# Performance work log

Measured on AMD Instinct MI355X. Metric: run time of the kernel, lower is better.

## Reference

```python
import jax, jax.numpy as jnp
import numpy as np

B, H, W, C = 16, 48, 48, 256
D_INNER = 2 * C          # ssm_ratio = 2.0
D_STATE = 1
DT_RANK = C // 16        # mamba convention: dt_rank = d_model // 16
HID = 4 * C              # mlp_ratio = 4.0
N = H * W


def _grid_neighbors(h, w):
    idx = np.arange(h * w).reshape(h, w)
    pad_r = -np.ones((1, w), np.int64)
    pad_c = -np.ones((h, 1), np.int64)
    up = np.concatenate([pad_r, idx[:-1]], 0)
    down = np.concatenate([idx[1:], pad_r], 0)
    left = np.concatenate([pad_c, idx[:, :-1]], 1)
    right = np.concatenate([idx[:, 1:], pad_c], 1)
    nb = np.stack([up, down, left, right], -1).reshape(h * w, 4)
    valid = nb >= 0
    return jnp.asarray(np.where(valid, nb, 0), np.int32), jnp.asarray(valid)

_NBR, _VALID = _grid_neighbors(H, W)


def _mst(x):
    """Input-adaptive MST (Prim) on the 4-connected pixel grid.
    Edge weight = exp(1 - cosine_similarity) between adjacent pixel features.
    Returns (order, par): Prim insertion order (a valid BFS-like topological order:
    every node's parent appears earlier) and parent node id per node."""
    b = x.shape[0]
    f = x.reshape(b, N, C)
    f = f / (jnp.linalg.norm(f, axis=-1, keepdims=True) + 1e-8)
    cos = jnp.einsum('bnc,bnkc->bnk', f, f[:, _NBR])          # (B,N,4)
    wgt = jnp.where(_VALID, jnp.exp(1.0 - cos), jnp.inf)

    def prim(wb):
        key = jnp.full((N,), jnp.inf, wb.dtype).at[0].set(0.0)
        par = jnp.zeros((N,), jnp.int32)
        intree = jnp.zeros((N,), bool)

        def step(carry, _):
            key, par, intree = carry
            u = jnp.argmin(jnp.where(intree, jnp.inf, key)).astype(jnp.int32)
            intree = intree.at[u].set(True)
            nb, wv = _NBR[u], wb[u]
            better = (~intree[nb]) & (wv < key[nb])
            key = key.at[nb].set(jnp.where(better, wv, key[nb]))
            par = par.at[nb].set(jnp.where(better, u, par[nb]))
            return (key, par, intree), u

        (_, par, _), order = jax.lax.scan(step, (key, par, intree), None, length=N)
        return order, par

    return jax.vmap(prim)(wgt)


def _ln(x, g, b):
    m = jnp.mean(x, -1, keepdims=True)
    v = jnp.var(x, -1, keepdims=True)
    return (x - m) * jax.lax.rsqrt(v + 1e-5) * g + b


def _tree_ssm(xn, order, par, W_in, b_in, W_xp, W_dt, b_dt, A_log, Dp, W_out, b_out):
    """Mamba-style selective scan generalized to a tree: the hidden state of node v
    recurses from its MST parent instead of the previous sequence position."""
    b = xn.shape[0]
    xf = xn.reshape(b, N, C)
    xz = xf @ W_in + b_in                               # (B,N,2*D_INNER)
    xi, z = xz[..., :D_INNER], xz[..., D_INNER:]
    xi = jax.nn.silu(xi)
    dbc = xi @ W_xp                                     # (B,N,DT_RANK+2)
    dtr = dbc[..., :DT_RANK]
    Bv = dbc[..., DT_RANK:DT_RANK + 1]                  # d_state = 1
    Cv = dbc[..., DT_RANK + 1:DT_RANK + 2]
    dt = jax.nn.softplus(dtr @ W_dt + b_dt)             # (B,N,D_INNER)
    A = -jnp.exp(A_log)                                 # (D_INNER,)
    decay = jnp.exp(dt * A)
    Bx = dt * Bv * xi

    def tree_scan(ob, pb, db, xb):
        def step(hbuf, v):
            hv = db[v] * hbuf[pb[v]] + xb[v]            # h[v] = decay*h[parent] + B*x
            return hbuf.at[v].set(hv), None
        hbuf, _ = jax.lax.scan(step, jnp.zeros((N, D_INNER), db.dtype), ob)
        return hbuf

    h = jax.vmap(tree_scan)(order, par, decay, Bx)      # (B,N,D_INNER)
    y = Cv * h + Dp * xi
    return ((y * jax.nn.silu(z)) @ W_out + b_out).reshape(xn.shape)


def setup_inputs():
    key = jax.random.key(0)
    ks = jax.random.split(key, 8)
    g = lambda k, shp, s=0.02: jax.random.normal(k, shp, jnp.float32) * s
    return {
        "x": jax.random.normal(ks[0], (B, H, W, C), jnp.float32),
        "norm1_w": jnp.ones((C,), jnp.float32), "norm1_b": jnp.zeros((C,), jnp.float32),
        "norm2_w": jnp.ones((C,), jnp.float32), "norm2_b": jnp.zeros((C,), jnp.float32),
        "W_in": g(ks[1], (C, 2 * D_INNER)), "b_in": jnp.zeros((2 * D_INNER,), jnp.float32),
        "W_xp": g(ks[2], (D_INNER, DT_RANK + 2 * D_STATE)),
        "W_dt": g(ks[3], (DT_RANK, D_INNER), 0.1), "b_dt": jnp.full((D_INNER,), -2.0, jnp.float32),
        "A_log": jnp.zeros((D_INNER,), jnp.float32), "Dp": jnp.ones((D_INNER,), jnp.float32),
        "W_out": g(ks[4], (D_INNER, C)), "b_out": jnp.zeros((C,), jnp.float32),
        "fc1_w": g(ks[5], (C, HID)), "fc1_b": jnp.zeros((HID,), jnp.float32),
        "fc2_w": g(ks[6], (HID, C)), "fc2_b": jnp.zeros((C,), jnp.float32),
    }


def reference(x, norm1_w, norm1_b, norm2_w, norm2_b, W_in, b_in, W_xp, W_dt, b_dt,
              A_log, Dp, W_out, b_out, fc1_w, fc1_b, fc2_w, fc2_b):
    order, par = _mst(jax.lax.stop_gradient(x))         # torch.no_grad() MST
    x = x + _tree_ssm(_ln(x, norm1_w, norm1_b), order, par,
                      W_in, b_in, W_xp, W_dt, b_dt, A_log, Dp, W_out, b_out)
    h = jax.nn.gelu(_ln(x, norm2_w, norm2_b) @ fc1_w + fc1_b, approximate=False)
    return x + h @ fc2_w + fc2_b
```

## Files before the change

### kernel.cpp

```cpp
#include <hip/hip_runtime.h>
#include <math.h>

#define NN 2304
#define BB 16
#define CC 256
#define DI 512
#define MM (BB*NN)

typedef __attribute__((ext_vector_type(8))) short bf16x8;
typedef __attribute__((ext_vector_type(4))) float f32x4;

__device__ inline unsigned short f2b(float f){
  unsigned u = __float_as_uint(f);
  u = u + 0x7FFFu + ((u>>16)&1u);
  return (unsigned short)(u>>16);
}
__device__ inline float b2f(unsigned short s){ return __uint_as_float(((unsigned)s)<<16); }
__device__ __forceinline__ int dstep(int d){ return (d==0)?-48:(d==1)?48:(d==2)?-1:1; }

__global__ __launch_bounds__(256) void k_prep(const float* __restrict__ W_in, const float* __restrict__ W_out,
    const float* __restrict__ fc1_w, const float* __restrict__ fc2_w, const float* __restrict__ W_xp,
    unsigned short* __restrict__ WinT, unsigned short* __restrict__ WoutT,
    unsigned short* __restrict__ fc1T, unsigned short* __restrict__ fc2T, float* __restrict__ WxpT)
{
  int idx = blockIdx.x*256 + threadIdx.x;
  if (idx < 262144){ int r=idx>>10, c=idx&1023; WinT[(size_t)c*256 + r] = f2b(W_in[idx]); return; }
  idx -= 262144;
  if (idx < 131072){ int r=idx>>8, c=idx&255; WoutT[(size_t)c*512 + r] = f2b(W_out[idx]); return; }
  idx -= 131072;
  if (idx < 262144){ int r=idx>>10, c=idx&1023; fc1T[(size_t)c*256 + r] = f2b(fc1_w[idx]); return; }
  idx -= 262144;
  if (idx < 262144){ int r=idx>>8, c=idx&255; fc2T[(size_t)c*1024 + r] = f2b(fc2_w[idx]); return; }
  idx -= 262144;
  if (idx < 9216){ int r=idx/18, c=idx-r*18; WxpT[(size_t)c*512 + r] = W_xp[idx]; }
}

__global__ __launch_bounds__(256) void k_normln(const float* __restrict__ xin, const float* __restrict__ g,
    const float* __restrict__ bta, float* __restrict__ innorm, unsigned short* __restrict__ outb)
{
  int row = blockIdx.x*4 + (threadIdx.x>>6); int lane=threadIdx.x&63;
  float4 v = *(const float4*)(xin + (size_t)row*CC + lane*4);
  float sq = v.x*v.x + v.y*v.y + v.z*v.z + v.w*v.w;
  float s  = v.x+v.y+v.z+v.w;
  #pragma unroll
  for (int o=32;o;o>>=1){ sq += __shfl_xor(sq,o); s += __shfl_xor(s,o); }
  if (lane==0) innorm[row] = 1.0f/(sqrtf(sq)+1e-8f);
  float m = s*(1.0f/256.0f);
  float dx=v.x-m, dy=v.y-m, dz=v.z-m, dw=v.w-m;
  float ss=dx*dx+dy*dy+dz*dz+dw*dw;
  #pragma unroll
  for (int o=32;o;o>>=1) ss += __shfl_xor(ss,o);
  float rs = rsqrtf(ss*(1.0f/256.0f)+1e-5f);
  int cb=lane*4;
  unsigned o0 = (unsigned)f2b(dx*rs*g[cb+0]+bta[cb+0]) | ((unsigned)f2b(dy*rs*g[cb+1]+bta[cb+1])<<16);
  unsigned o1 = (unsigned)f2b(dz*rs*g[cb+2]+bta[cb+2]) | ((unsigned)f2b(dw*rs*g[cb+3]+bta[cb+3])<<16);
  *(uint2*)(outb + (size_t)row*CC + cb) = make_uint2(o0,o1);
}

__global__ __launch_bounds__(256) void k_edge(const float* __restrict__ x, const float* __restrict__ innorm, float* __restrict__ wgt){
  int g = blockIdx.x*4 + (threadIdx.x>>6); int lane = threadIdx.x&63;
  int b = g/NN, n = g - b*NN;
  int r = n/48, c = n - (n/48)*48;
  const float* xb = x + ((size_t)b*NN)*CC;
  float4 vu = *(const float4*)(xb + (size_t)n*CC + lane*4);
  int nb0=(r>0)?n-48:-1, nb1=(r<47)?n+48:-1, nb2=(c>0)?n-1:-1, nb3=(c<47)?n+1:-1;
  float d0=0,d1=0,d2=0,d3=0;
  if (nb0>=0){ float4 t=*(const float4*)(xb+(size_t)nb0*CC+lane*4); d0=vu.x*t.x+vu.y*t.y+vu.z*t.z+vu.w*t.w; }
  if (nb1>=0){ float4 t=*(const float4*)(xb+(size_t)nb1*CC+lane*4); d1=vu.x*t.x+vu.y*t.y+vu.z*t.z+vu.w*t.w; }
  if (nb2>=0){ float4 t=*(const float4*)(xb+(size_t)nb2*CC+lane*4); d2=vu.x*t.x+vu.y*t.y+vu.z*t.z+vu.w*t.w; }
  if (nb3>=0){ float4 t=*(const float4*)(xb+(size_t)nb3*CC+lane*4); d3=vu.x*t.x+vu.y*t.y+vu.z*t.z+vu.w*t.w; }
  #pragma unroll
  for (int o=32;o;o>>=1){ d0+=__shfl_xor(d0,o); d1+=__shfl_xor(d1,o); d2+=__shfl_xor(d2,o); d3+=__shfl_xor(d3,o); }
  if (lane==0){
    float inu = innorm[g];
    float inf_ = __uint_as_float(0x7F800000u);
    float4 w;
    w.x = (nb0>=0)? expf(1.0f - d0*(inu*innorm[g-n+nb0])) : inf_;
    w.y = (nb1>=0)? expf(1.0f - d1*(inu*innorm[g-n+nb1])) : inf_;
    w.z = (nb2>=0)? expf(1.0f - d2*(inu*innorm[g-n+nb2])) : inf_;
    w.w = (nb3>=0)? expf(1.0f - d3*(inu*innorm[g-n+nb3])) : inf_;
    *(float4*)(wgt + (size_t)g*4) = w;
  }
}

#define INFB 0x7F800000u
#define NILA 0x3FFFu
__device__ void mst_body(unsigned char* smem, const float* __restrict__ wgt, int b,
    unsigned short* __restrict__ parpos_g, int* __restrict__ lvlorder,
    int* __restrict__ lvlstart, int* __restrict__ nlvl)
{
  unsigned* tmask = (unsigned*)smem;
  unsigned* pk    = (unsigned*)(smem + 9216);
  unsigned* comp   = pk;
  unsigned* bestw  = pk + 2304;
  unsigned* bestid = pk + 4608;
  unsigned short* par   = (unsigned short*)(smem + 46080);
  unsigned short* dpos  = (unsigned short*)(smem + 50688);
  int* hist = (int*)(smem + 55296);
  int* ctr  = (int*)(smem + 64512);
  const int tid = threadIdx.x;
  const float* wb = wgt + (size_t)b*NN*4;

  #pragma unroll
  for (int k=0;k<9;k++){ int v=tid+k*256; comp[v]=v; tmask[v]=0u; }
  __syncthreads();

  for (int round=0; round<14; round++){
    #pragma unroll
    for (int k=0;k<9;k++){ int v=tid+k*256; bestw[v]=INFB; bestid[v]=0xFFFFFFFFu; }
    __syncthreads();
    unsigned candw[9], candi[9];
    #pragma unroll
    for (int k=0;k<9;k++){
      int v=tid+k*256;
      unsigned cv=comp[v];
      int r=v/48, c=v-(v/48)*48;
      float4 w4 = *(const float4*)(wb + (size_t)v*4);
      unsigned cw=INFB, ci=0xFFFFFFFFu;
      if (r>0  && comp[v-48]!=cv){ unsigned wv=__float_as_uint(w4.x); if (wv<cw){cw=wv;ci=(unsigned)(v*4+0);} }
      if (r<47 && comp[v+48]!=cv){ unsigned wv=__float_as_uint(w4.y); if (wv<cw){cw=wv;ci=(unsigned)(v*4+1);} }
      if (c>0  && comp[v-1] !=cv){ unsigned wv=__float_as_uint(w4.z); if (wv<cw){cw=wv;ci=(unsigned)(v*4+2);} }
      if (c<47 && comp[v+1] !=cv){ unsigned wv=__float_as_uint(w4.w); if (wv<cw){cw=wv;ci=(unsigned)(v*4+3);} }
      candw[k]=cw; candi[k]=ci;
      if (cw!=INFB) atomicMin(&bestw[cv], cw);
    }
    __syncthreads();
    #pragma unroll
    for (int k=0;k<9;k++){
      if (candw[k]!=INFB){
        int v=tid+k*256; unsigned cv=comp[v];
        if (bestw[cv]==candw[k]) atomicMin(&bestid[cv], candi[k]);
      }
    }
    __syncthreads();
    unsigned hookS[9];
    #pragma unroll
    for (int k=0;k<9;k++){
      int v=tid+k*256; hookS[k]=0xFFFFFFFFu;
      if (comp[v]!=(unsigned)v) continue;
      unsigned id=bestid[v];
      if (id==0xFFFFFFFFu) continue;
      int u=(int)(id>>2), d=(int)(id&3);
      int o = u + dstep(d);
      unsigned s = comp[o];
      unsigned sid = bestid[s];
      bool mutual=false;
      if (sid!=0xFFFFFFFFu){
        int su=(int)(sid>>2), sd=(int)(sid&3);
        int so = su + dstep(sd);
        mutual = (comp[so]==(unsigned)v);
      }
      if (!mutual || (unsigned)v>s) hookS[k]=s;
    }
    __syncthreads();
    #pragma unroll
    for (int k=0;k<9;k++){
      if (hookS[k]==0xFFFFFFFFu) continue;
      int v=tid+k*256;
      unsigned id=bestid[v];
      int u=(int)(id>>2), d=(int)(id&3);
      int o = u + dstep(d);
      comp[v]=hookS[k];
      atomicOr(&tmask[u], 1u<<d);
      atomicOr(&tmask[o], 1u<<(d^1));
    }
    __syncthreads();
    for (int it=0; it<16; it++){
      if (tid==0) ctr[1]=0;
      __syncthreads();
      int ch=0;
      #pragma unroll
      for (int k=0;k<9;k++){
        int v=tid+k*256;
        unsigned c1=comp[v], c2=comp[c1];
        if (c1!=c2){ comp[v]=c2; ch=1; }
      }
      if (ch) atomicAdd(&ctr[1],1);
      __syncthreads();
      if (ctr[1]==0) break;
    }
    if (tid==0) ctr[2]=0;
    __syncthreads();
    int rc=0;
    #pragma unroll
    for (int k=0;k<9;k++){ int v=tid+k*256; if (comp[v]==(unsigned)v) rc++; }
    if (rc) atomicAdd(&ctr[2], rc);
    __syncthreads();
    if (ctr[2]<=1) break;
  }
  __syncthreads();

  int a0;
  { unsigned m0 = tmask[0]; a0 = __ffs((int)(m0&0xFu))-1; }

  for (int pass=0; pass<2; pass++){
    for (int k=0;k<36;k++){
      int a = k*256+tid;
      int v = a>>2, d = a&3;
      unsigned mv = tmask[v];
      unsigned sc = NILA;
      unsigned vl = pass ? 8192u : 0u;
      if ((mv>>d)&1u){
        int w = v + dstep(d);
        unsigned mw = tmask[w];
        int rd = d^1;
        int nd = -1;
        #pragma unroll
        for (int kk=1;kk<=4;kk++){ int c2=(rd+kk)&3; if (nd<0 && ((mw>>c2)&1u)) nd=c2; }
        sc = (unsigned)(w*4+nd);
        if (sc==(unsigned)a0) sc=NILA;
        vl = pass ? (8192u + (((mv>>(4+d))&1u)? 1u : (unsigned)-1)) : 1u;
      }
      pk[a] = (sc<<14) | (vl & 0x3FFFu);
    }
    __syncthreads();
    for (int it=0; it<13; it++){
      unsigned stg[36];
      #pragma unroll
      for (int k=0;k<36;k++){
        int a=k*256+tid;
        unsigned mine=pk[a];
        unsigned s=mine>>14;
        if (s==NILA) stg[k]=mine;
        else {
          unsigned oth=pk[s];
          unsigned nv=(mine&0x3FFFu)+(oth&0x3FFFu);
          if (pass) nv -= 8192u;
          stg[k]=((oth>>14)<<14)|(nv&0x3FFFu);
        }
      }
      __syncthreads();
      #pragma unroll
      for (int k=0;k<36;k++) pk[k*256+tid]=stg[k];
      __syncthreads();
    }
    if (pass==0){
      for (int k=0;k<36;k++){
        int a=k*256+tid;
        int v=a>>2, d=a&3;
        if ((tmask[v]>>d)&1u){
          int w=v+dstep(d);
          int ra=w*4+(d^1);
          if ((pk[a]&0x3FFFu) > (pk[ra]&0x3FFFu)){
            atomicOr(&tmask[v], 16u<<d);
            par[w]=(unsigned short)v;
          }
        }
      }
      __syncthreads();
    }
  }
  if (tid==0){ par[0]=0; dpos[0]=0; ctr[3]=0; }
  __syncthreads();
  for (int k=0;k<36;k++){
    int a=k*256+tid;
    int v=a>>2, d=a&3;
    unsigned mv=tmask[v];
    if (((mv>>d)&1u) && ((mv>>(4+d))&1u)){
      int w=v+dstep(d);
      int S=(int)(pk[a]&0x3FFFu)-8192;
      int dep=1-S;
      dpos[w]=(unsigned short)dep;
      atomicMax(&ctr[3],dep);
    }
  }
  __syncthreads();
  int nlv_=ctr[3]+1;
  for (int i=tid;i<nlv_;i+=256) hist[i]=0;
  __syncthreads();
  for (int i=tid;i<NN;i+=256) atomicAdd(&hist[dpos[i]],1);
  __syncthreads();
  if (tid==0){
    int run=0;
    for (int l=0;l<nlv_;l++){ int c2=hist[l]; hist[l]=run; lvlstart[b*(NN+2)+l]=run; run+=c2; }
    lvlstart[b*(NN+2)+nlv_]=run;
    nlvl[b]=nlv_;
  }
  __syncthreads();
  for (int i=tid;i<NN;i+=256){
    int pos=atomicAdd(&hist[dpos[i]],1);
    lvlorder[b*NN+pos]=i;
    dpos[i]=(unsigned short)pos;
  }
  __syncthreads();
  for (int i=tid;i<NN;i+=256)
    parpos_g[b*NN + dpos[i]] = dpos[par[i]];
}

template<int EPI>
__device__ void gemm_body(unsigned short* lA, unsigned short* lB, int bm, int bn,
    const unsigned short* __restrict__ A, const unsigned short* __restrict__ BT,
    const float* __restrict__ bias, int Ndim, int K,
    const float* __restrict__ addin, float* __restrict__ fout,
    unsigned short* __restrict__ bout0, unsigned short* __restrict__ bout1,
    const int* __restrict__ lvl)
{
  int tid=threadIdx.x, wid=tid>>6, lane=tid&63;
  const unsigned short* Ab = A + (size_t)bm*128*K;
  const unsigned short* Bb = BT + (size_t)bn*128*K;
  int wr=wid>>1, wc=wid&1;
  f32x4 acc[4][4];
  #pragma unroll
  for (int m2=0;m2<4;m2++)
    #pragma unroll
    for (int n2=0;n2<4;n2++)
      #pragma unroll
      for (int j=0;j<4;j++) acc[m2][n2][j]=0.f;
  int r0 = tid>>2, c0 = (tid&3)*8;
  for (int k0=0;k0<K;k0+=32){
    int4 va0 = *(const int4*)(Ab + (size_t)r0*K + k0 + c0);
    int4 va1 = *(const int4*)(Ab + (size_t)(r0+64)*K + k0 + c0);
    int4 vb0 = *(const int4*)(Bb + (size_t)r0*K + k0 + c0);
    int4 vb1 = *(const int4*)(Bb + (size_t)(r0+64)*K + k0 + c0);
    __syncthreads();
    *(int4*)(lA + r0*32 + c0) = va0;
    *(int4*)(lA + (r0+64)*32 + c0) = va1;
    *(int4*)(lB + r0*32 + c0) = vb0;
    *(int4*)(lB + (r0+64)*32 + c0) = vb1;
    __syncthreads();
    int ra = (wr<<6) + (lane&15);
    int rb = (wc<<6) + (lane&15);
    int cb = (lane>>4)<<3;
    bf16x8 af[4], bfr[4];
    #pragma unroll
    for (int m2=0;m2<4;m2++) af[m2] = *(const bf16x8*)(lA + (ra+m2*16)*32 + cb);
    #pragma unroll
    for (int n2=0;n2<4;n2++) bfr[n2] = *(const bf16x8*)(lB + (rb+n2*16)*32 + cb);
    #pragma unroll
    for (int m2=0;m2<4;m2++)
      #pragma unroll
      for (int n2=0;n2<4;n2++)
        acc[m2][n2] = __builtin_amdgcn_mfma_f32_16x16x32_bf16(af[m2], bfr[n2], acc[m2][n2], 0,0,0);
  }
  int rr = (lane>>4)<<2, cc = lane&15;
  #pragma unroll
  for (int m2=0;m2<4;m2++){
    #pragma unroll
    for (int n2=0;n2<4;n2++){
      int col = (bn<<7) + (wc<<6) + (n2<<4) + cc;
      float bs = bias[col];
      #pragma unroll
      for (int j=0;j<4;j++){
        int row = (bm<<7) + (wr<<6) + (m2<<4) + rr + j;
        float v = acc[m2][n2][j] + bs;
        if (EPI==0){
          float sv = v * (1.0f/(1.0f+expf(-v)));
          if (col < DI) bout0[(size_t)row*DI + col] = f2b(sv);
          else          bout1[(size_t)row*DI + col - DI] = f2b(sv);
        } else if (EPI==1){
          size_t oi=(size_t)row*Ndim+col;
          fout[oi] = addin[oi] + v;
        } else if (EPI==2){
          size_t oi=(size_t)row*Ndim+col;
          bout0[oi] = f2b(0.5f*v*(1.0f+erff(v*0.70710678118f)));
        } else if (EPI==3){
          int grow = (row/NN)*NN + lvl[row];
          fout[(size_t)row*Ndim+col] = addin[(size_t)grow*Ndim+col] + v;
        } else {
          int grow = (row/NN)*NN + lvl[row];
          fout[(size_t)grow*Ndim+col] = addin[(size_t)row*Ndim+col] + v;
        }
      }
    }
  }
}

template<int EPI>
__global__ __launch_bounds__(256) void k_gemm(
    const unsigned short* __restrict__ A, const unsigned short* __restrict__ BT,
    const float* __restrict__ bias, int Ndim, int K,
    const float* __restrict__ addin, float* __restrict__ fout,
    unsigned short* __restrict__ bout0, unsigned short* __restrict__ bout1,
    const int* __restrict__ lvl)
{
  __shared__ __align__(16) unsigned short lAB[128*32*2];
  int ntn = Ndim>>7;
  int bm = blockIdx.x/ntn, bn = blockIdx.x - bm*ntn;
  gemm_body<EPI>(lAB, lAB+128*32, bm, bn, A, BT, bias, Ndim, K, addin, fout, bout0, bout1, lvl);
}

__global__ __launch_bounds__(256) void k_fused(
    const unsigned short* __restrict__ xn, const unsigned short* __restrict__ WinT,
    const float* __restrict__ b_in,
    unsigned short* __restrict__ xi_b, unsigned short* __restrict__ sz_b,
    const float* __restrict__ wgt, unsigned short* __restrict__ parpos_g,
    int* __restrict__ lvlorder, int* __restrict__ lvlstart, int* __restrict__ nlvl)
{
  __shared__ __align__(16) unsigned char smem[64528];
  if (blockIdx.x < BB){
    mst_body(smem, wgt, blockIdx.x, parpos_g, lvlorder, lvlstart, nlvl);
  } else {
    int bid = blockIdx.x - BB;
    int bm = bid>>3, bn = bid&7;
    gemm_body<0>((unsigned short*)smem, (unsigned short*)smem + 128*32, bm, bn,
                 xn, WinT, b_in, 1024, 256, nullptr, nullptr, xi_b, sz_b, nullptr);
  }
}

__global__ __launch_bounds__(256) void k_ln(const float* __restrict__ xin, const float* __restrict__ g,
    const float* __restrict__ bta, unsigned short* __restrict__ outb)
{
  int row = blockIdx.x*4 + (threadIdx.x>>6); int lane=threadIdx.x&63;
  float4 v = *(const float4*)(xin + (size_t)row*CC + lane*4);
  float s = v.x+v.y+v.z+v.w;
  #pragma unroll
  for (int o=32;o;o>>=1) s += __shfl_xor(s,o);
  float m = s*(1.0f/256.0f);
  float dx=v.x-m, dy=v.y-m, dz=v.z-m, dw=v.w-m;
  float ss=dx*dx+dy*dy+dz*dz+dw*dw;
  #pragma unroll
  for (int o=32;o;o>>=1) ss += __shfl_xor(ss,o);
  float rs = rsqrtf(ss*(1.0f/256.0f)+1e-5f);
  int cb=lane*4;
  unsigned o0 = (unsigned)f2b(dx*rs*g[cb+0]+bta[cb+0]) | ((unsigned)f2b(dy*rs*g[cb+1]+bta[cb+1])<<16);
  unsigned o1 = (unsigned)f2b(dz*rs*g[cb+2]+bta[cb+2]) | ((unsigned)f2b(dw*rs*g[cb+3]+bta[cb+3])<<16);
  *(uint2*)(outb + (size_t)row*CC + cb) = make_uint2(o0,o1);
}

__global__ __launch_bounds__(256) void k_dbc(const unsigned short* __restrict__ xi_b,
    const float* __restrict__ WxpT, float* __restrict__ dbc)
{
  int row = blockIdx.x*4 + (threadIdx.x>>6); int lane=threadIdx.x&63;
  int4 raw = *(const int4*)(xi_b + (size_t)row*DI + lane*8);
  float xf[8];
  xf[0]=b2f((unsigned short)((unsigned)raw.x&0xFFFFu)); xf[1]=b2f((unsigned short)((unsigned)raw.x>>16));
  xf[2]=b2f((unsigned short)((unsigned)raw.y&0xFFFFu)); xf[3]=b2f((unsigned short)((unsigned)raw.y>>16));
  xf[4]=b2f((unsigned short)((unsigned)raw.z&0xFFFFu)); xf[5]=b2f((unsigned short)((unsigned)raw.z>>16));
  xf[6]=b2f((unsigned short)((unsigned)raw.w&0xFFFFu)); xf[7]=b2f((unsigned short)((unsigned)raw.w>>16));
  for (int jc=0;jc<18;jc++){
    const float* wr_ = WxpT + (size_t)jc*DI + lane*8;
    float s=0.f;
    #pragma unroll
    for (int t=0;t<8;t++) s += xf[t]*wr_[t];
    #pragma unroll
    for (int o=32;o;o>>=1) s += __shfl_xor(s,o);
    if (lane==0) dbc[(size_t)row*18+jc]=s;
  }
}

__global__ __launch_bounds__(512) void k_dbx(const float* __restrict__ dbc, const unsigned short* __restrict__ xi_b,
  const float* __restrict__ W_dt, const float* __restrict__ b_dt, const float* __restrict__ A_log,
  const int* __restrict__ lvlorder,
  unsigned short* __restrict__ dec_cm, unsigned short* __restrict__ bx_cm)
{
  __shared__ int smap[32];
  __shared__ float sd[32][18];
  int c = threadIdx.x;
  int b = blockIdx.x/72, pg = blockIdx.x - b*72;
  int p0 = pg*32;
  if (c<32) smap[c] = b*NN + lvlorder[b*NN + p0 + c];
  __syncthreads();
  for (int i=c;i<32*18;i+=512){ int rr=i/18, q=i-rr*18; sd[rr][q]=dbc[(size_t)smap[rr]*18+q]; }
  __syncthreads();
  float wdt[16];
  #pragma unroll
  for (int r2=0;r2<16;r2++) wdt[r2]=W_dt[r2*DI+c];
  float bd=b_dt[c];
  float nA=-expf(A_log[c]);
  unsigned decp[16], bxp[16];
  #pragma unroll
  for (int rr=0;rr<32;rr++){
    float a=bd;
    #pragma unroll
    for (int r2=0;r2<16;r2++) a += sd[rr][r2]*wdt[r2];
    float dt = (a>20.f)? a : log1pf(expf(a));
    float dec = expf(dt*nA);
    float bx = dt*sd[rr][16]*b2f(xi_b[(size_t)smap[rr]*DI + c]);
    if (rr&1){ decp[rr>>1] |= ((unsigned)f2b(dec))<<16; bxp[rr>>1] |= ((unsigned)f2b(bx))<<16; }
    else     { decp[rr>>1]  =  (unsigned)f2b(dec);      bxp[rr>>1]  =  (unsigned)f2b(bx); }
  }
  size_t chb = ((size_t)b*DI + c)*NN + p0;
  uint4* dp = (uint4*)(dec_cm + chb);
  uint4* bp = (uint4*)(bx_cm + chb);
  #pragma unroll
  for (int q=0;q<4;q++){
    uint4 dv, bv;
    dv.x=decp[q*4+0]; dv.y=decp[q*4+1]; dv.z=decp[q*4+2]; dv.w=decp[q*4+3];
    bv.x=bxp[q*4+0];  bv.y=bxp[q*4+1];  bv.z=bxp[q*4+2];  bv.w=bxp[q*4+3];
    dp[q]=dv; bp[q]=bv;
  }
}

#define SCH 4
__global__ __launch_bounds__(256) void k_scan(const unsigned short* __restrict__ dec_cm,
    unsigned short* __restrict__ bx_cm,
    const unsigned short* __restrict__ parpos_g,
    const int* __restrict__ lvlstart, const int* __restrict__ nlvl)
{
  __shared__ unsigned short sdec[SCH*NN];
  __shared__ unsigned short sbx[SCH*NN];
  __shared__ unsigned short spp[NN];
  int b = blockIdx.x>>7, t = blockIdx.x&127;
  int c0 = t*SCH;
  int tid = threadIdx.x;
  const size_t gch = ((size_t)b*DI + c0)*NN;
  #pragma unroll
  for (int cc=0;cc<SCH;cc++){
    const uint2* gd = (const uint2*)(dec_cm + gch + (size_t)cc*NN);
    const uint2* gb = (const uint2*)(bx_cm + gch + (size_t)cc*NN);
    uint2* ld = (uint2*)(sdec + cc*NN);
    uint2* lb = (uint2*)(sbx + cc*NN);
    for (int i=tid;i<NN/4;i+=256){ ld[i]=gd[i]; lb[i]=gb[i]; }
  }
  for (int i=tid;i<NN;i+=256) spp[i]=parpos_g[b*NN+i];
  int nlv = nlvl[b];
  __syncthreads();
  for (int lvl=1; lvl<nlv; lvl++){
    int s=lvlstart[b*(NN+2)+lvl], e=lvlstart[b*(NN+2)+lvl+1];
    int tot=(e-s)*SCH;
    for (int idx=tid; idx<tot; idx+=256){
      int p = s + (idx>>2);
      int cc = idx&3;
      int pp = spp[p];
      float hv = b2f(sdec[cc*NN+p])*b2f(sbx[cc*NN+pp]) + b2f(sbx[cc*NN+p]);
      sbx[cc*NN+p] = f2b(hv);
    }
    __syncthreads();
  }
  #pragma unroll
  for (int cc=0;cc<SCH;cc++){
    uint2* gb = (uint2*)(bx_cm + gch + (size_t)cc*NN);
    const uint2* lb = (const uint2*)(sbx + cc*NN);
    for (int i=tid;i<NN/4;i+=256) gb[i]=lb[i];
  }
}

__global__ __launch_bounds__(512) void k_u(const unsigned short* __restrict__ h_cm,
    const unsigned short* __restrict__ xi_b, const unsigned short* __restrict__ sz_b,
    const float* __restrict__ dbc, const float* __restrict__ Dp,
    const int* __restrict__ lvlorder, unsigned short* __restrict__ u_perm)
{
  __shared__ int smap[32];
  __shared__ unsigned short hT[32*512];
  int c = threadIdx.x;
  int b = blockIdx.x/72, pg = blockIdx.x - b*72;
  int p0 = pg*32;
  if (c<32) smap[c] = b*NN + lvlorder[b*NN + p0 + c];
  {
    const uint4* gh = (const uint4*)(h_cm + ((size_t)b*DI + c)*NN + p0);
    #pragma unroll
    for (int q=0;q<4;q++){
      uint4 w = gh[q];
      unsigned ws[4] = {w.x,w.y,w.z,w.w};
      #pragma unroll
      for (int e=0;e<4;e++){
        hT[(q*8+e*2+0)*512 + c] = (unsigned short)(ws[e]&0xFFFFu);
        hT[(q*8+e*2+1)*512 + c] = (unsigned short)(ws[e]>>16);
      }
    }
  }
  float dpc = Dp[c];
  __syncthreads();
  #pragma unroll 4
  for (int rr=0;rr<32;rr++){
    int grow = smap[rr];
    float Cv = dbc[(size_t)grow*18+17];
    float xiv = b2f(xi_b[(size_t)grow*DI + c]);
    float szv = b2f(sz_b[(size_t)grow*DI + c]);
    float hv = b2f(hT[rr*512 + c]);
    float u = (Cv*hv + dpc*xiv)*szv;
    u_perm[((size_t)(b*NN + p0 + rr))*DI + c] = f2b(u);
  }
}

extern "C" void kernel_launch(void* const* d_in, const int* in_sizes, int n_in,
                              void* d_out, int out_size, void* d_ws, size_t ws_size,
                              hipStream_t stream) {
  (void)in_sizes; (void)n_in; (void)out_size; (void)ws_size;
  const float* x      = (const float*)d_in[0];
  const float* n1w    = (const float*)d_in[1];
  const float* n1b    = (const float*)d_in[2];
  const float* n2w    = (const float*)d_in[3];
  const float* n2b    = (const float*)d_in[4];
  const float* W_in   = (const float*)d_in[5];
  const float* b_in   = (const float*)d_in[6];
  const float* W_xp   = (const float*)d_in[7];
  const float* W_dt   = (const float*)d_in[8];
  const float* b_dt   = (const float*)d_in[9];
  const float* A_log  = (const float*)d_in[10];
  const float* Dp     = (const float*)d_in[11];
  const float* W_out  = (const float*)d_in[12];
  const float* b_out  = (const float*)d_in[13];
  const float* fc1_w  = (const float*)d_in[14];
  const float* fc1_b  = (const float*)d_in[15];
  const float* fc2_w  = (const float*)d_in[16];
  const float* fc2_b  = (const float*)d_in[17];

  char* base=(char*)d_ws; size_t off=0;
  auto alc=[&](size_t nb)->char*{ char* p=base+off; off=(off+nb+255)&~(size_t)255; return p; };
  float* wgt            = (float*)alc((size_t)MM*4*4);
  float* innorm         = (float*)alc((size_t)MM*4);
  unsigned short* parpos= (unsigned short*)alc((size_t)MM*2);
  int* lvlorder         = (int*)alc((size_t)MM*4);
  int* lvlstart         = (int*)alc((size_t)BB*(NN+2)*4);
  int* nlvl             = (int*)alc((size_t)BB*4);
  unsigned short* xi_b  = (unsigned short*)alc((size_t)MM*DI*2);
  unsigned short* sz_b  = (unsigned short*)alc((size_t)MM*DI*2);
  float* dbc            = (float*)alc((size_t)MM*18*4);
  unsigned short* dec_cm= (unsigned short*)alc((size_t)MM*DI*2);
  unsigned short* bx_cm = (unsigned short*)alc((size_t)MM*DI*2);
  unsigned short* WinT  = (unsigned short*)alc((size_t)CC*1024*2);
  unsigned short* WoutT = (unsigned short*)alc((size_t)DI*CC*2);
  unsigned short* fc1T  = (unsigned short*)alc((size_t)CC*1024*2);
  unsigned short* fc2T  = (unsigned short*)alc((size_t)1024*CC*2);
  float* WxpT           = (float*)alc((size_t)DI*18*4);
  unsigned short* xn      = (unsigned short*)dec_cm;
  unsigned short* h_cm    = bx_cm;
  unsigned short* u_perm  = dec_cm;
  float* x2_perm          = (float*)bx_cm;
  unsigned short* x2n_perm= dec_cm;
  unsigned short* g1_perm = xi_b;

  k_prep<<<dim3(3620),dim3(256),0,stream>>>(W_in, W_out, fc1_w, fc2_w, W_xp,
                                            WinT, WoutT, fc1T, fc2T, WxpT);
  k_normln<<<dim3(MM/4),dim3(256),0,stream>>>(x, n1w, n1b, innorm, xn);
  k_edge<<<dim3(MM/4),dim3(256),0,stream>>>(x, innorm, wgt);

  k_fused<<<dim3(BB + 288*8),dim3(256),0,stream>>>(xn, WinT, b_in, xi_b, sz_b,
                                                   wgt, parpos, lvlorder, lvlstart, nlvl);

  k_dbc<<<dim3(MM/4),dim3(256),0,stream>>>(xi_b, WxpT, dbc);
  k_dbx<<<dim3(MM/32),dim3(512),0,stream>>>(dbc, xi_b, W_dt, b_dt, A_log, lvlorder, dec_cm, bx_cm);
  k_scan<<<dim3(BB*128),dim3(256),0,stream>>>(dec_cm, bx_cm, parpos, lvlstart, nlvl);
  k_u<<<dim3(MM/32),dim3(512),0,stream>>>(h_cm, xi_b, sz_b, dbc, Dp, lvlorder, u_perm);

  k_gemm<3><<<dim3(288*2),dim3(256),0,stream>>>(u_perm, WoutT, b_out, 256, 512,
                                                x, x2_perm, nullptr, nullptr, lvlorder);
  k_ln<<<dim3(MM/4),dim3(256),0,stream>>>(x2_perm, n2w, n2b, x2n_perm);
  k_gemm<2><<<dim3(288*8),dim3(256),0,stream>>>(x2n_perm, fc1T, fc1_b, 1024, 256,
                                                nullptr, nullptr, g1_perm, nullptr, nullptr);
  k_gemm<4><<<dim3(288*2),dim3(256),0,stream>>>(g1_perm, fc2T, fc2_b, 256, 1024,
                                                x2_perm, (float*)d_out, nullptr, nullptr, lvlorder);
}
```

Baseline: 711.8 us.

## Double GEMM K-tile with padded LDS and trim Boruvka loop barriers

The GEMM body now stages 64-wide K tiles instead of 32, using an LDS row stride of 72 elements. This halves the number of barrier-separated load/store rounds and the padding reduces LDS bank conflicts on the fragment reads. The MST Boruvka loop now uses __syncthreads_count in place of shared-counter atomics plus extra barriers. It exits when no component hooks rather than counting roots, which removes several syncs per iteration. LDS use grows to about 36KB per GEMM block, which may reduce occupancy.

New measurement: 888.2 us. 1.25x slower.

```diff
diff --git a/kernel.cpp b/kernel.cpp
--- a/kernel.cpp
+++ b/kernel.cpp
@@ -6,6 +6,7 @@
 #define CC 256
 #define DI 512
 #define MM (BB*NN)
+#define LDK 72
 
 typedef __attribute__((ext_vector_type(8))) short bf16x8;
 typedef __attribute__((ext_vector_type(4))) float f32x4;
@@ -134,6 +135,7 @@
     }
     __syncthreads();
     unsigned hookS[9];
+    int hooked = 0;
     #pragma unroll
     for (int k=0;k<9;k++){
       int v=tid+k*256; hookS[k]=0xFFFFFFFFu;
@@ -150,7 +152,7 @@
         int so = su + dstep(sd);
         mutual = (comp[so]==(unsigned)v);
       }
-      if (!mutual || (unsigned)v>s) hookS[k]=s;
+      if (!mutual || (unsigned)v>s){ hookS[k]=s; hooked=1; }
     }
     __syncthreads();
     #pragma unroll
@@ -164,10 +166,8 @@
       atomicOr(&tmask[u], 1u<<d);
       atomicOr(&tmask[o], 1u<<(d^1));
     }
-    __syncthreads();
+    if (__syncthreads_count(hooked)==0) break;
     for (int it=0; it<16; it++){
-      if (tid==0) ctr[1]=0;
-      __syncthreads();
       int ch=0;
       #pragma unroll
       for (int k=0;k<9;k++){
@@ -175,18 +175,8 @@
         unsigned c1=comp[v], c2=comp[c1];
         if (c1!=c2){ comp[v]=c2; ch=1; }
       }
-      if (ch) atomicAdd(&ctr[1],1);
-      __syncthreads();
-      if (ctr[1]==0) break;
-    }
-    if (tid==0) ctr[2]=0;
-    __syncthreads();
-    int rc=0;
-    #pragma unroll
-    for (int k=0;k<9;k++){ int v=tid+k*256; if (comp[v]==(unsigned)v) rc++; }
-    if (rc) atomicAdd(&ctr[2], rc);
-    __syncthreads();
-    if (ctr[2]<=1) break;
+      if (__syncthreads_count(ch)==0) break;
+    }
   }
   __syncthreads();
 
@@ -306,31 +296,38 @@
     for (int n2=0;n2<4;n2++)
       #pragma unroll
       for (int j=0;j<4;j++) acc[m2][n2][j]=0.f;
-  int r0 = tid>>2, c0 = (tid&3)*8;
-  for (int k0=0;k0<K;k0+=32){
-    int4 va0 = *(const int4*)(Ab + (size_t)r0*K + k0 + c0);
-    int4 va1 = *(const int4*)(Ab + (size_t)(r0+64)*K + k0 + c0);
-    int4 vb0 = *(const int4*)(Bb + (size_t)r0*K + k0 + c0);
-    int4 vb1 = *(const int4*)(Bb + (size_t)(r0+64)*K + k0 + c0);
-    __syncthreads();
-    *(int4*)(lA + r0*32 + c0) = va0;
-    *(int4*)(lA + (r0+64)*32 + c0) = va1;
-    *(int4*)(lB + r0*32 + c0) = vb0;
-    *(int4*)(lB + (r0+64)*32 + c0) = vb1;
-    __syncthreads();
-    int ra = (wr<<6) + (lane&15);
-    int rb = (wc<<6) + (lane&15);
-    int cb = (lane>>4)<<3;
-    bf16x8 af[4], bfr[4];
-    #pragma unroll
-    for (int m2=0;m2<4;m2++) af[m2] = *(const bf16x8*)(lA + (ra+m2*16)*32 + cb);
-    #pragma unroll
-    for (int n2=0;n2<4;n2++) bfr[n2] = *(const bf16x8*)(lB + (rb+n2*16)*32 + cb);
-    #pragma unroll
-    for (int m2=0;m2<4;m2++)
-      #pragma unroll
-      for (int n2=0;n2<4;n2++)
-        acc[m2][n2] = __builtin_amdgcn_mfma_f32_16x16x32_bf16(af[m2], bfr[n2], acc[m2][n2], 0,0,0);
+  int r0 = tid>>3;
+  int c0 = (tid&7)*8;
+  int ra = (wr<<6) + (lane&15);
+  int rb = (wc<<6) + (lane&15);
+  int cb = (lane>>4)<<3;
+  for (int k0=0;k0<K;k0+=64){
+    int4 va[4], vb[4];
+    #pragma unroll
+    for (int q=0;q<4;q++){
+      va[q] = *(const int4*)(Ab + (size_t)(r0+q*32)*K + k0 + c0);
+      vb[q] = *(const int4*)(Bb + (size_t)(r0+q*32)*K + k0 + c0);
+    }
+    __syncthreads();
+    #pragma unroll
+    for (int q=0;q<4;q++){
+      *(int4*)(lA + (r0+q*32)*LDK + c0) = va[q];
+      *(int4*)(lB + (r0+q*32)*LDK + c0) = vb[q];
+    }
+    __syncthreads();
+    #pragma unroll
+    for (int kk=0;kk<64;kk+=32){
+      bf16x8 af[4], bfr[4];
+      #pragma unroll
+      for (int m2=0;m2<4;m2++) af[m2] = *(const bf16x8*)(lA + (ra+m2*16)*LDK + kk + cb);
+      #pragma unroll
+      for (int n2=0;n2<4;n2++) bfr[n2] = *(const bf16x8*)(lB + (rb+n2*16)*LDK + kk + cb);
+      #pragma unroll
+      for (int m2=0;m2<4;m2++)
+        #pragma unroll
+        for (int n2=0;n2<4;n2++)
+          acc[m2][n2] = __builtin_amdgcn_mfma_f32_16x16x32_bf16(af[m2], bfr[n2], acc[m2][n2], 0,0,0);
+    }
   }
   int rr = (lane>>4)<<2, cc = lane&15;
   #pragma unroll
@@ -373,10 +370,10 @@
     unsigned short* __restrict__ bout0, unsigned short* __restrict__ bout1,
     const int* __restrict__ lvl)
 {
-  __shared__ __align__(16) unsigned short lAB[128*32*2];
+  __shared__ __align__(16) unsigned short lAB[128*LDK*2];
   int ntn = Ndim>>7;
   int bm = blockIdx.x/ntn, bn = blockIdx.x - bm*ntn;
-  gemm_body<EPI>(lAB, lAB+128*32, bm, bn, A, BT, bias, Ndim, K, addin, fout, bout0, bout1, lvl);
+  gemm_body<EPI>(lAB, lAB+128*LDK, bm, bn, A, BT, bias, Ndim, K, addin, fout, bout0, bout1, lvl);
 }
 
 __global__ __launch_bounds__(256) void k_fused(
@@ -392,7 +389,7 @@
   } else {
     int bid = blockIdx.x - BB;
     int bm = bid>>3, bn = bid&7;
-    gemm_body<0>((unsigned short*)smem, (unsigned short*)smem + 128*32, bm, bn,
+    gemm_body<0>((unsigned short*)smem, (unsigned short*)smem + 128*LDK, bm, bn,
                  xn, WinT, b_in, 1024, 256, nullptr, nullptr, xi_b, sz_b, nullptr);
   }
 }
```
